# Kernel tuning notes

Measured on AMD Instinct MI355X. Metric: run time of the kernel, lower is better.

Reference implementation:

```python
import jax, jax.numpy as jnp
import numpy as np

B, D_IN, U, E = 8192, 1024, 1024, 16

def setup_inputs() -> dict:
    key = jax.random.key(0)
    k1, k2, k3, k4 = jax.random.split(key, 4)
    inputs = jax.random.normal(k1, (B, D_IN), dtype=jnp.float32)
    # type_prob: probability over entity types per example, [B, E, 1]
    tp = jax.random.uniform(k2, (B, E, 1), dtype=jnp.float32)
    type_prob = tp / jnp.sum(tp, axis=1, keepdims=True)
    # Stacked per-entity Dense params: W [E, D_IN, U], b [E, U]
    scale = 1.0 / np.sqrt(D_IN)
    W = jax.random.normal(k3, (E, D_IN, U), dtype=jnp.float32) * scale
    b = jax.random.normal(k4, (E, U), dtype=jnp.float32) * 0.01
    return {"inputs": inputs, "type_prob": type_prob, "W": W, "b": b}

def reference(inputs, type_prob, W, b):
    # Per-entity Dense, batched as one einsum: [B, E, U]
    logits = jnp.einsum('bd,edu->beu', inputs, W) + b
    probs = jax.nn.softmax(logits, axis=-1)  # softmax over wp_units, per entity
    # transpose to [B, U, E], matmul with type_prob [B, E, 1], reduce_sum last axis
    # == weighted combine over entities: [B, U]
    result = jnp.einsum('beu,be->bu', probs, type_prob[..., 0])
    return result
```

## Files before the change

kernel.cpp:

```cpp
#include <hip/hip_runtime.h>
#include <hip/hip_bf16.h>
#include <hip/hip_fp16.h>
#include <stdint.h>

typedef _Float16 f16;
typedef _Float16 f16x4 __attribute__((ext_vector_type(4)));
typedef _Float16 f16x8 __attribute__((ext_vector_type(8)));
typedef float f32x4 __attribute__((ext_vector_type(4)));

#define NB 8192
#define ND 1024
#define NU 1024
#define NE 16

__global__ __launch_bounds__(256) void k_prep(const float* __restrict__ W,
                                              f16* __restrict__ WT,
                                              const float* __restrict__ X,
                                              f16* __restrict__ Xh) {
  const int bid = blockIdx.x;
  const int t = threadIdx.x;
  if (bid < 4096) {
    __shared__ f16 tile[64][68];
    const int u0 = (bid & 15) * 64;
    const int d0 = ((bid >> 4) & 15) * 64;
    const int e = bid >> 8;
    const int r = t >> 4;
    const int c = (t & 15) << 2;
    const float* src = W + (size_t)e * ND * NU;
    f16* dst = WT + (size_t)e * NU * ND;
#pragma unroll
    for (int i = 0; i < 4; ++i) {
      const int rr = r + i * 16;
      const float4 v = *(const float4*)(src + (size_t)(d0 + rr) * NU + (u0 + c));
      tile[rr][c + 0] = (f16)v.x;
      tile[rr][c + 1] = (f16)v.y;
      tile[rr][c + 2] = (f16)v.z;
      tile[rr][c + 3] = (f16)v.w;
    }
    __syncthreads();
#pragma unroll
    for (int i = 0; i < 4; ++i) {
      const int rr = r + i * 16;
      f16x4 h;
      h[0] = tile[c + 0][rr];
      h[1] = tile[c + 1][rr];
      h[2] = tile[c + 2][rr];
      h[3] = tile[c + 3][rr];
      *(f16x4*)(dst + (size_t)(u0 + rr) * ND + (d0 + c)) = h;
    }
  } else {
    const size_t i = ((size_t)(bid - 4096) * 256 + t) * 8;
    const float4 v0 = *(const float4*)(X + i);
    const float4 v1 = *(const float4*)(X + i + 4);
    f16x8 h;
    h[0] = (f16)v0.x; h[1] = (f16)v0.y; h[2] = (f16)v0.z; h[3] = (f16)v0.w;
    h[4] = (f16)v1.x; h[5] = (f16)v1.y; h[6] = (f16)v1.z; h[7] = (f16)v1.w;
    *(f16x8*)(Xh + i) = h;
  }
}


typedef __attribute__((address_space(3))) void lds_void_t;
typedef __attribute__((address_space(1))) const void gbl_void_t;

__device__ __forceinline__ void gload16(const void* g, void* l) {
  __builtin_amdgcn_global_load_lds((gbl_void_t*)g, (lds_void_t*)l, 16, 0, 0);
}

#define WAIT_VM8() do { asm volatile("s_waitcnt vmcnt(8)" ::: "memory"); \
                        __builtin_amdgcn_sched_barrier(0); } while (0)
#define WAIT_LGKM0() do { asm volatile("s_waitcnt lgkmcnt(0)" ::: "memory"); \
                          __builtin_amdgcn_sched_barrier(0); } while (0)
#define BARR() do { asm volatile("" ::: "memory"); __builtin_amdgcn_s_barrier(); \
                    asm volatile("" ::: "memory"); } while (0)

#define STAGEA(srcp, h, kl, buf)                                                \
  {                                                                             \
    _Pragma("unroll") for (int i_ = 0; i_ < 2; ++i_) {                          \
      const unsigned s_ = i_ * 512 + t;                                         \
      const unsigned row_ = (h) * 128 + (s_ >> 3);                              \
      const unsigned sch_ = (s_ & 7) ^ (row_ & 7);                              \
      const unsigned lb_ = (unsigned)(buf) * 32768 + (h) * 16384 +              \
                           (i_ * 512 + (t & ~63u)) * 16;                        \
      gload16((srcp) + (size_t)row_ * 2048 + (size_t)(kl) * 128 + sch_ * 16,    \
              smem + lb_);                                                      \
    }                                                                           \
  }

#define LDA(mb0, buf)                                                           \
  _Pragma("unroll") for (int j_ = 0; j_ < 4; ++j_)                              \
    _Pragma("unroll") for (int ks_ = 0; ks_ < 2; ++ks_)                         \
      a[j_][ks_] = *(const f16x8*)(smem + (unsigned)(buf) * 32768 +             \
                     (wr * 128 + ((mb0) + j_) * 16 + ln) * 128 +                \
                     (((unsigned)(ks_ * 4 + g)) ^ (ln & 7u)) * 16);

#define BLOAD2(n0, kl)                                                          \
  _Pragma("unroll") for (int n_ = (n0); n_ < (n0) + 2; ++n_)                    \
    _Pragma("unroll") for (int ks_ = 0; ks_ < 2; ++ks_)                         \
      b[n_][ks_] = *(const f16x8*)(Bg + (size_t)(wc * 64 + n_ * 16 + ln) * 2048 \
                     + (size_t)(kl) * 128 + (unsigned)(ks_ * 4 + g) * 16);

#define QUAD(mb0, n0)                                                           \
  _Pragma("unroll") for (int j_ = 0; j_ < 4; ++j_)                              \
    _Pragma("unroll") for (int n_ = 0; n_ < 2; ++n_)                            \
      _Pragma("unroll") for (int ks_ = 0; ks_ < 2; ++ks_)                       \
        acc[(mb0) + j_][(n0) + n_] = __builtin_amdgcn_mfma_f32_16x16x32_f16(    \
            a[j_][ks_], b[(n0) + n_][ks_], acc[(mb0) + j_][(n0) + n_], 0, 0, 0);

__global__ __launch_bounds__(512, 2) void k_gemm_exp(const f16* __restrict__ Xc,
                                                     const f16* __restrict__ WT,
                                                     const float* __restrict__ BIAS,
                                                     f16* __restrict__ P,
                                                     float* __restrict__ S4,
                                                     int TPB, int CR) {
  __shared__ alignas(16) unsigned char smem[65536 + 4096];
  float* red = (float*)(smem + 65536);

  const int t = threadIdx.x;
  const int w = t >> 6;
  const int l = t & 63;
  const int g = l >> 4;
  const int ln = l & 15;
  const int wr = w >> 2;
  const int wc = w & 3;

  const int bid = blockIdx.x;
  const int xcd = bid & 7;
  const int i = bid >> 3;
  const int ntl = i >> 2;
  const int q = i & 3;
  const int nt = xcd * 8 + ntl;
  const int mt0 = q * TPB;

  const char* Xc0 = (const char*)Xc;
  const char* Bg = (const char*)WT + (size_t)nt * 256 * 2048;

  f32x4 acc[8][4];
#pragma unroll
  for (int mb = 0; mb < 8; ++mb)
#pragma unroll
    for (int nb = 0; nb < 4; ++nb) acc[mb][nb] = (f32x4){0.f, 0.f, 0.f, 0.f};

  f16x8 a[4][2], b[4][2];

  float bv[4];
  const float* bp = BIAS + ((size_t)(nt >> 2) << 10) + (nt & 3) * 256 + wc * 64 + ln;
#pragma unroll
  for (int nb = 0; nb < 4; ++nb) bv[nb] = bp[nb * 16];

  const int TOT = TPB * 16;

  {
    const char* Ag0 = Xc0 + (size_t)mt0 * 256 * 2048;
    STAGEA(Ag0, 0, 0, 0);
    STAGEA(Ag0, 1, 0, 0);
    __builtin_amdgcn_sched_barrier(0);
    BLOAD2(0, 0);
    BLOAD2(2, 0);
    WAIT_VM8();
    BARR();
  }

#pragma unroll 1
  for (int kt = 0; kt < TOT; ++kt) {
    const int cur = kt & 1, nxt = cur ^ 1;
    const int ti = kt >> 4;
    const bool lastk = (kt == TOT - 1);
    const int kt1 = lastk ? kt : kt + 1;
    const int t1 = kt1 >> 4, kl1 = kt1 & 15;
    const char* Ag1 = Xc0 + (size_t)(mt0 + t1) * 256 * 2048;

    LDA(0, cur);
    if (!lastk) {
      STAGEA(Ag1, 0, kl1, nxt);
      STAGEA(Ag1, 1, kl1, nxt);
    }
    __builtin_amdgcn_sched_barrier(0);
    __builtin_amdgcn_s_setprio(1);
    QUAD(0, 0);
    QUAD(0, 2);
    __builtin_amdgcn_s_setprio(0);
    LDA(4, cur);
    __builtin_amdgcn_s_setprio(1);
    QUAD(4, 0);
    __builtin_amdgcn_s_setprio(0);
    if (!lastk) BLOAD2(0, kl1);
    __builtin_amdgcn_s_setprio(1);
    QUAD(4, 2);
    __builtin_amdgcn_s_setprio(0);
    if (!lastk) {
      BLOAD2(2, kl1);
      WAIT_VM8();
    }
    BARR();

    if ((kt & 15) == 15) {
      const int mt = mt0 + ti;
      f16* Prow =
          P + (size_t)(mt * 256 + wr * 128) * 16384 + (size_t)nt * 256 + wc * 64 + ln;
#pragma unroll
      for (int mb = 0; mb < 8; ++mb) {
        float rs[4] = {0.f, 0.f, 0.f, 0.f};
#pragma unroll
        for (int nb = 0; nb < 4; ++nb) {
#pragma unroll
          for (int r = 0; r < 4; ++r) {
            const float p = __expf(acc[mb][nb][r] + bv[nb]);
            rs[r] += p;
            Prow[(size_t)(mb * 16 + g * 4 + r) * 16384 + nb * 16] = (f16)p;
            acc[mb][nb][r] = 0.f;
          }
        }
#pragma unroll
        for (int r = 0; r < 4; ++r) {
          float v = rs[r];
          v += __shfl_xor(v, 1);
          v += __shfl_xor(v, 2);
          v += __shfl_xor(v, 4);
          v += __shfl_xor(v, 8);
          if (ln == 0) red[(wr * 128 + mb * 16 + g * 4 + r) * 4 + wc] = v;
        }
      }
      WAIT_LGKM0();
      BARR();
      if (t < 256) {
        const float s =
            (red[t * 4 + 0] + red[t * 4 + 1]) + (red[t * 4 + 2] + red[t * 4 + 3]);
        S4[(size_t)nt * CR + mt * 256 + t] = s;
      }
      BARR();
    }
  }
}

__global__ __launch_bounds__(512) void k_combine(const f16* __restrict__ P,
                                                 const float* __restrict__ TP,
                                                 const float* __restrict__ S4,
                                                 float* __restrict__ OUT,
                                                 int RB, int CR) {
  __shared__ float c_s[4][16];
  const int t = threadIdx.x;
  const int blk = blockIdx.x;
  if (t < 64) {
    const int rr = t >> 4, e = t & 15;
    const int bl = blk * 4 + rr;
    float S = 0.f;
#pragma unroll
    for (int q = 0; q < 4; ++q) S += S4[(size_t)(e * 4 + q) * CR + bl];
    c_s[rr][e] = TP[(size_t)(RB + bl) * NE + e] / S;
  }
  __syncthreads();
  const int rl = t >> 7;
  const int bl = blk * 4 + rl;
  const int u0 = (t & 127) * 8;
  float acm[8] = {0.f, 0.f, 0.f, 0.f, 0.f, 0.f, 0.f, 0.f};
  const f16* Pb = P + (size_t)bl * 16384 + u0;
#pragma unroll
  for (int e = 0; e < NE; ++e) {
    const float c = c_s[rl][e];
    const f16x8 pv = *(const f16x8*)(Pb + e * 1024);
#pragma unroll
    for (int jj = 0; jj < 8; ++jj) acm[jj] += c * (float)pv[jj];
  }
  float* op = OUT + (size_t)(RB + bl) * NU + u0;
  *(float4*)(op) = (float4){acm[0], acm[1], acm[2], acm[3]};
  *(float4*)(op + 4) = (float4){acm[4], acm[5], acm[6], acm[7]};
}

#define BM 64
#define BUH 512
#define NRT 128
#define WT_BYTES ((size_t)NE * NU * ND * 2)
#define SUMS_FLOATS ((size_t)NE * NRT * 2 * 64)
#define FLG_INTS ((size_t)NE * NRT * 2)

#define LOADB(F, soff)                                   \
  {                                                      \
    const char* p_ = wtc + (soff) + vbase;               \
    F[0] = *(const f16x8*)(p_);                          \
    F[1] = *(const f16x8*)(p_ + 1 * 16 * ND * 2);        \
    F[2] = *(const f16x8*)(p_ + 2 * 16 * ND * 2);        \
    F[3] = *(const f16x8*)(p_ + 3 * 16 * ND * 2);        \
  }

#define MFMA_HALF(F, kbyte)                                                         \
  {                                                                                 \
    const f16x8 a0 = *(const f16x8*)(A_s + (ln + 0) * 2064 + g * 16 + (kbyte));     \
    const f16x8 a1 = *(const f16x8*)(A_s + (ln + 16) * 2064 + g * 16 + (kbyte));    \
    const f16x8 a2 = *(const f16x8*)(A_s + (ln + 32) * 2064 + g * 16 + (kbyte));    \
    const f16x8 a3 = *(const f16x8*)(A_s + (ln + 48) * 2064 + g * 16 + (kbyte));    \
    _Pragma("unroll") for (int n_ = 0; n_ < 4; ++n_) {                              \
      acc[0][n_] = __builtin_amdgcn_mfma_f32_16x16x32_f16(a0, F[n_], acc[0][n_], 0, 0, 0); \
      acc[1][n_] = __builtin_amdgcn_mfma_f32_16x16x32_f16(a1, F[n_], acc[1][n_], 0, 0, 0); \
      acc[2][n_] = __builtin_amdgcn_mfma_f32_16x16x32_f16(a2, F[n_], acc[2][n_], 0, 0, 0); \
      acc[3][n_] = __builtin_amdgcn_mfma_f32_16x16x32_f16(a3, F[n_], acc[3][n_], 0, 0, 0); \
    }                                                                               \
  }

__device__ __forceinline__ size_t wt_soff(int L) {
  L = (L > 511) ? 511 : L;
  return (size_t)(L >> 5) * ((size_t)NU * ND * 2) + (size_t)(L & 31) * 64;
}

__global__ __launch_bounds__(512, 2) void k_proj(const float* __restrict__ X,
                                                 const float* __restrict__ TP,
                                                 const f16* __restrict__ WT,
                                                 const float* __restrict__ BIAS,
                                                 float* __restrict__ OUT,
                                                 float* __restrict__ SUMS,
                                                 int* __restrict__ FLG) {
  __shared__ alignas(16) unsigned char lds[132096 + 4096 + 2048 + 256];
  unsigned char* A_s = lds;
  float* tp_s = (float*)(lds + 132096);
  float* reds = (float*)(lds + 132096 + 4096);
  float* sums_s = (float*)(lds + 132096 + 4096 + 2048);

  const int t = threadIdx.x;
  const int w = t >> 6;
  const int l = t & 63;
  const int g = l >> 4;
  const int ln = l & 15;
  const int bid = blockIdx.x;
  const int rt = bid >> 1;
  const int uh = bid & 1;
  const int b0 = rt * BM;
  const int c0 = uh * BUH;

#pragma unroll
  for (int i = 0; i < 32; ++i) {
    const int idx = (i * 512 + t) << 2;
    const int row = idx >> 10;
    const int col = idx & 1023;
    const float4 v = *(const float4*)(X + (size_t)(b0 + row) * ND + col);
    f16x4 h;
    h[0] = (f16)v.x; h[1] = (f16)v.y; h[2] = (f16)v.z; h[3] = (f16)v.w;
    *(f16x4*)(A_s + row * 2064 + (col << 1)) = h;
  }
  tp_s[t] = TP[(size_t)(b0 + (t >> 4)) * NE + (t & 15)];
  tp_s[512 + t] = TP[(size_t)(b0 + 32 + (t >> 4)) * NE + (t & 15)];
  __syncthreads();

  f32x4 out_acc[4][4];
#pragma unroll
  for (int m = 0; m < 4; ++m)
#pragma unroll
    for (int n = 0; n < 4; ++n) out_acc[m][n] = (f32x4){0.f, 0.f, 0.f, 0.f};

  const char* wtc = (const char*)WT;
  const unsigned vbase = ((unsigned)(c0 + w * 64 + ln) * ND + g * 8) * 2;

  f16x8 F0[4], F1[4], F2[4], F3[4];
  LOADB(F0, wt_soff(0));
  LOADB(F1, wt_soff(1));
  LOADB(F2, wt_soff(2));

  for (int e = 0; e < NE; ++e) {
    f32x4 acc[4][4];
#pragma unroll
    for (int m = 0; m < 4; ++m)
#pragma unroll
      for (int n = 0; n < 4; ++n) acc[m][n] = (f32x4){0.f, 0.f, 0.f, 0.f};

    const int Le = e * 32;
#pragma unroll 1
    for (int gi = 0; gi < 7; ++gi) {
      const int L = Le + gi * 4;
      const int kb = gi * 4 * 64;
      LOADB(F3, wt_soff(L + 3));
      MFMA_HALF(F0, kb + 0);
      LOADB(F0, wt_soff(L + 4));
      MFMA_HALF(F1, kb + 64);
      LOADB(F1, wt_soff(L + 5));
      MFMA_HALF(F2, kb + 128);
      LOADB(F2, wt_soff(L + 6));
      MFMA_HALF(F3, kb + 192);
    }
    LOADB(F3, wt_soff(Le + 31));
    MFMA_HALF(F0, 28 * 64);
    LOADB(F0, wt_soff(Le + 32));
    MFMA_HALF(F1, 29 * 64);
    LOADB(F1, wt_soff(Le + 33));
    MFMA_HALF(F2, 30 * 64);
    LOADB(F2, wt_soff(Le + 34));
    MFMA_HALF(F3, 31 * 64);

    const float* bp = BIAS + (size_t)e * NU + c0 + w * 64 + ln;
    float bv[4];
#pragma unroll
    for (int n = 0; n < 4; ++n) bv[n] = bp[n * 16];

    float rs[4][4];
#pragma unroll
    for (int m = 0; m < 4; ++m)
#pragma unroll
      for (int r = 0; r < 4; ++r) rs[m][r] = 0.f;
#pragma unroll
    for (int m = 0; m < 4; ++m)
#pragma unroll
      for (int n = 0; n < 4; ++n)
#pragma unroll
        for (int r = 0; r < 4; ++r) {
          const float p = __expf(acc[m][n][r] + bv[n]);
          acc[m][n][r] = p;
          rs[m][r] += p;
        }
#pragma unroll
    for (int m = 0; m < 4; ++m)
#pragma unroll
      for (int r = 0; r < 4; ++r) {
        float v = rs[m][r];
        v += __shfl_xor(v, 1, 64);
        v += __shfl_xor(v, 2, 64);
        v += __shfl_xor(v, 4, 64);
        v += __shfl_xor(v, 8, 64);
        rs[m][r] = v;
      }
    if (ln == 0) {
#pragma unroll
      for (int m = 0; m < 4; ++m)
#pragma unroll
        for (int r = 0; r < 4; ++r) reds[(m * 16 + g * 4 + r) * 8 + w] = rs[m][r];
    }
    __syncthreads();

    const int pairbase = (e * NRT + rt) * 2;
    float myS = 0.f;
    if (t < 64) {
      const float* rp = reds + t * 8;
      myS = ((rp[0] + rp[1]) + (rp[2] + rp[3])) + ((rp[4] + rp[5]) + (rp[6] + rp[7]));
      __hip_atomic_store(&SUMS[(size_t)(pairbase + uh) * 64 + t], myS,
                         __ATOMIC_RELAXED, __HIP_MEMORY_SCOPE_AGENT);
    }
    __syncthreads();
    if (t == 0) {
      __threadfence();
      __hip_atomic_store(&FLG[pairbase + uh], 1, __ATOMIC_RELEASE, __HIP_MEMORY_SCOPE_AGENT);
      int spin = 0;
      while (__hip_atomic_load(&FLG[pairbase + (uh ^ 1)], __ATOMIC_ACQUIRE,
                               __HIP_MEMORY_SCOPE_AGENT) == 0 &&
             spin < 400000) {
        __builtin_amdgcn_s_sleep(2);
        ++spin;
      }
    }
    __syncthreads();
    if (t < 64) {
      const float ps = __hip_atomic_load(&SUMS[(size_t)(pairbase + (uh ^ 1)) * 64 + t],
                                         __ATOMIC_RELAXED, __HIP_MEMORY_SCOPE_AGENT);
      sums_s[t] = myS + ps;
    }
    __syncthreads();

#pragma unroll
    for (int m = 0; m < 4; ++m)
#pragma unroll
      for (int r = 0; r < 4; ++r) {
        const int row = m * 16 + g * 4 + r;
        const float scale = tp_s[row * 16 + e] * __builtin_amdgcn_rcpf(sums_s[row]);
#pragma unroll
        for (int n = 0; n < 4; ++n) out_acc[m][n][r] += scale * acc[m][n][r];
      }
  }

#pragma unroll
  for (int m = 0; m < 4; ++m)
#pragma unroll
    for (int r = 0; r < 4; ++r) {
      float* op = OUT + (size_t)(b0 + m * 16 + g * 4 + r) * NU + c0 + w * 64 + ln;
#pragma unroll
      for (int n = 0; n < 4; ++n) op[n * 16] = out_acc[m][n][r];
    }
}

extern "C" void kernel_launch(void* const* d_in, const int* in_sizes, int n_in,
                              void* d_out, int out_size, void* d_ws, size_t ws_size,
                              hipStream_t stream) {
  const float* X = (const float*)d_in[0];
  const float* TP = (const float*)d_in[1];
  const float* W = (const float*)d_in[2];
  const float* BIAS = (const float*)d_in[3];
  float* OUT = (float*)d_out;

  const size_t XH_BYTES = (size_t)NB * ND * 2;
  const size_t FIXED = WT_BYTES + XH_BYTES;

  int CR = 0;
  for (int cr = NB; cr >= 1024; cr >>= 1) {
    const size_t need = FIXED + (size_t)cr * 16384 * 2 + (size_t)cr * 64 * 4;
    if (ws_size >= need) { CR = cr; break; }
  }

  if (CR > 0) {
    f16* WT = (f16*)d_ws;
    f16* Xh = (f16*)((char*)d_ws + WT_BYTES);
    float* S4 = (float*)((char*)d_ws + FIXED);
    f16* P = (f16*)((char*)d_ws + FIXED + (size_t)CR * 64 * 4);

    k_prep<<<dim3(8192), dim3(256), 0, stream>>>(W, WT, X, Xh);

    const int MT = CR / 256;
    const int TPB = MT / 4;
    const int nch = NB / CR;
    for (int ch = 0; ch < nch; ++ch) {
      const int RB = ch * CR;
      k_gemm_exp<<<dim3(256), dim3(512), 0, stream>>>(
          (const f16*)((const char*)Xh + (size_t)RB * ND * 2), WT, BIAS, P, S4, TPB, CR);
      k_combine<<<dim3(CR / 4), dim3(512), 0, stream>>>(P, TP, S4, OUT, RB, CR);
    }
  } else {
    f16* WT = (f16*)d_ws;
    float* SUMS = (float*)((char*)d_ws + WT_BYTES);
    int* FLG = (int*)((char*)d_ws + WT_BYTES + SUMS_FLOATS * 4);

    hipMemsetAsync(FLG, 0, FLG_INTS * sizeof(int), stream);
    k_prep<<<dim3(4096), dim3(256), 0, stream>>>(W, WT, X, nullptr);
    k_proj<<<dim3(256), dim3(512), 0, stream>>>(X, TP, WT, BIAS, OUT, SUMS, FLG);
  }
}
```

Baseline: 461.8 us.

## Stage B tiles through LDS with deeper ping-pong pipeline and interleaved barriers

B (weight) tiles are now staged into LDS with direct global-to-LDS loads instead of being read straight from global memory into registers. The LDS buffer doubles to 128KB and the main loop is unrolled by two with ping-pong buffers. Loads are prefetched two k-steps ahead and split into chunks interleaved between MFMA quads, separated by barriers. This aims to hide global latency and get coalesced B reads, but it adds many barriers per step and enough LDS use to limit occupancy.

```diff
diff --git a/kernel.cpp b/kernel.cpp
--- a/kernel.cpp
+++ b/kernel.cpp
@@ -67,38 +67,31 @@
   __builtin_amdgcn_global_load_lds((gbl_void_t*)g, (lds_void_t*)l, 16, 0, 0);
 }
 
-#define WAIT_VM8() do { asm volatile("s_waitcnt vmcnt(8)" ::: "memory"); \
+#define WAIT_VM6() do { asm volatile("s_waitcnt vmcnt(6)" ::: "memory"); \
+                        __builtin_amdgcn_sched_barrier(0); } while (0)
+#define WAIT_VM0() do { asm volatile("s_waitcnt vmcnt(0)" ::: "memory"); \
                         __builtin_amdgcn_sched_barrier(0); } while (0)
 #define WAIT_LGKM0() do { asm volatile("s_waitcnt lgkmcnt(0)" ::: "memory"); \
                           __builtin_amdgcn_sched_barrier(0); } while (0)
 #define BARR() do { asm volatile("" ::: "memory"); __builtin_amdgcn_s_barrier(); \
                     asm volatile("" ::: "memory"); } while (0)
 
-#define STAGEA(srcp, h, kl, buf)                                                \
-  {                                                                             \
-    _Pragma("unroll") for (int i_ = 0; i_ < 2; ++i_) {                          \
-      const unsigned s_ = i_ * 512 + t;                                         \
-      const unsigned row_ = (h) * 128 + (s_ >> 3);                              \
-      const unsigned sch_ = (s_ & 7) ^ (row_ & 7);                              \
-      const unsigned lb_ = (unsigned)(buf) * 32768 + (h) * 16384 +              \
-                           (i_ * 512 + (t & ~63u)) * 16;                        \
-      gload16((srcp) + (size_t)row_ * 2048 + (size_t)(kl) * 128 + sch_ * 16,    \
-              smem + lb_);                                                      \
-    }                                                                           \
-  }
-
-#define LDA(mb0, buf)                                                           \
-  _Pragma("unroll") for (int j_ = 0; j_ < 4; ++j_)                              \
-    _Pragma("unroll") for (int ks_ = 0; ks_ < 2; ++ks_)                         \
-      a[j_][ks_] = *(const f16x8*)(smem + (unsigned)(buf) * 32768 +             \
-                     (wr * 128 + ((mb0) + j_) * 16 + ln) * 128 +                \
-                     (((unsigned)(ks_ * 4 + g)) ^ (ln & 7u)) * 16);
-
-#define BLOAD2(n0, kl)                                                          \
-  _Pragma("unroll") for (int n_ = (n0); n_ < (n0) + 2; ++n_)                    \
-    _Pragma("unroll") for (int ks_ = 0; ks_ < 2; ++ks_)                         \
-      b[n_][ks_] = *(const f16x8*)(Bg + (size_t)(wc * 64 + n_ * 16 + ln) * 2048 \
-                     + (size_t)(kl) * 128 + (unsigned)(ks_ * 4 + g) * 16);
+#define STG(srcp, op, h, kb, BUF)                                               \
+  { _Pragma("unroll") for (int i_ = 0; i_ < 2; ++i_)                            \
+      gload16((srcp) + (h) * 262144 + (size_t)(kb) + sOff[i_],                  \
+              smem + ((BUF) * 65536 + (op) * 32768 + (h) * 16384) + dOff[i_]); }
+
+#define LDA2(mb0, CB)                                                           \
+  _Pragma("unroll") for (int j_ = 0; j_ < 4; ++j_) {                            \
+    a[j_][0] = *(const f16x8*)(smem + A0b[CB] + ((mb0) + j_) * 2048);           \
+    a[j_][1] = *(const f16x8*)(smem + A1b[CB] + ((mb0) + j_) * 2048);           \
+  }
+
+#define LDB2(CB)                                                                \
+  _Pragma("unroll") for (int n_ = 0; n_ < 4; ++n_) {                            \
+    b[n_][0] = *(const f16x8*)(smem + B0b[CB] + n_ * 2048);                     \
+    b[n_][1] = *(const f16x8*)(smem + B1b[CB] + n_ * 2048);                     \
+  }
 
 #define QUAD(mb0, n0)                                                           \
   _Pragma("unroll") for (int j_ = 0; j_ < 4; ++j_)                              \
@@ -107,14 +100,49 @@
         acc[(mb0) + j_][(n0) + n_] = __builtin_amdgcn_mfma_f32_16x16x32_f16(    \
             a[j_][ks_], b[(n0) + n_][ks_], acc[(mb0) + j_][(n0) + n_], 0, 0, 0);
 
+#define KBODY(ktv, CB)                                                          \
+  {                                                                             \
+    const int kt_ = (ktv);                                                      \
+    const bool lastT_ = ((kt_ >> 4) == TPB - 1);                                \
+    const bool lastk_ = (kt_ == TOT - 1);                                       \
+    const bool sk14_ = lastT_ && ((kt_ & 15) >= 14);                            \
+    const int kt1_ = lastk_ ? kt_ : kt_ + 1;                                    \
+    const char* Ag1_ = Xc0 + (size_t)(mt0 + (kt1_ >> 4)) * 524288;              \
+    const int kb1_ = (kt1_ & 15) * 128;                                         \
+    const int kt2_ = (kt_ + 2 < TOT) ? kt_ + 2 : kt_;                           \
+    const char* Ag2_ = Xc0 + (size_t)(mt0 + (kt2_ >> 4)) * 524288;              \
+    const int kb2_ = (kt2_ & 15) * 128;                                         \
+    if (lastk_) { WAIT_VM0(); BARR(); }                                         \
+    LDA2(0, CB);                                                                \
+    LDB2(CB);                                                                   \
+    if (!lastk_) STG(Ag1_, 0, 1, kb1_, (CB) ^ 1);                               \
+    BARR();                                                                     \
+    __builtin_amdgcn_s_setprio(1); QUAD(0, 0); __builtin_amdgcn_s_setprio(0);   \
+    BARR();                                                                     \
+    if (!sk14_) STG(Bg, 1, 0, kb2_, CB);                                        \
+    BARR();                                                                     \
+    __builtin_amdgcn_s_setprio(1); QUAD(0, 2); __builtin_amdgcn_s_setprio(0);   \
+    BARR();                                                                     \
+    LDA2(4, CB);                                                                \
+    if (!sk14_) STG(Bg, 1, 1, kb2_, CB);                                        \
+    BARR();                                                                     \
+    __builtin_amdgcn_s_setprio(1); QUAD(4, 2); __builtin_amdgcn_s_setprio(0);   \
+    BARR();                                                                     \
+    if (!sk14_) STG(Ag2_, 0, 0, kb2_, CB);                                      \
+    BARR();                                                                     \
+    __builtin_amdgcn_s_setprio(1); QUAD(4, 0); __builtin_amdgcn_s_setprio(0);   \
+    if (!lastk_) WAIT_VM6();                                                    \
+    BARR();                                                                     \
+  }
+
 __global__ __launch_bounds__(512, 2) void k_gemm_exp(const f16* __restrict__ Xc,
                                                      const f16* __restrict__ WT,
                                                      const float* __restrict__ BIAS,
                                                      f16* __restrict__ P,
                                                      float* __restrict__ S4,
                                                      int TPB, int CR) {
-  __shared__ alignas(16) unsigned char smem[65536 + 4096];
-  float* red = (float*)(smem + 65536);
+  __shared__ alignas(16) unsigned char smem[131072 + 4096];
+  float* red = (float*)(smem + 131072);
 
   const int t = threadIdx.x;
   const int w = t >> 6;
@@ -133,7 +161,25 @@
   const int mt0 = q * TPB;
 
   const char* Xc0 = (const char*)Xc;
-  const char* Bg = (const char*)WT + (size_t)nt * 256 * 2048;
+  const char* Bg = (const char*)WT + (size_t)nt * 524288;
+
+  const unsigned aRow = (unsigned)(wr * 128 + ln) * 128;
+  const unsigned bRow = 32768u + (unsigned)(wc >> 1) * 16384 +
+                        (unsigned)((wc & 1) * 64 + ln) * 128;
+  const unsigned x0 = (unsigned)(g ^ (ln & 7)) * 16;
+  const unsigned x1 = (unsigned)((4 + g) ^ (ln & 7)) * 16;
+  const unsigned A0b[2] = {aRow + x0, aRow + x0 + 65536u};
+  const unsigned A1b[2] = {aRow + x1, aRow + x1 + 65536u};
+  const unsigned B0b[2] = {bRow + x0, bRow + x0 + 65536u};
+  const unsigned B1b[2] = {bRow + x1, bRow + x1 + 65536u};
+
+  unsigned sOff[2], dOff[2];
+#pragma unroll
+  for (int i_ = 0; i_ < 2; ++i_) {
+    const unsigned s_ = i_ * 512 + t;
+    sOff[i_] = (s_ >> 3) * 2048 + (((s_ & 7) ^ ((s_ >> 3) & 7)) * 16);
+    dOff[i_] = (i_ * 512 + (t & ~63u)) * 16;
+  }
 
   f32x4 acc[8][4];
 #pragma unroll
@@ -151,51 +197,25 @@
   const int TOT = TPB * 16;
 
   {
-    const char* Ag0 = Xc0 + (size_t)mt0 * 256 * 2048;
-    STAGEA(Ag0, 0, 0, 0);
-    STAGEA(Ag0, 1, 0, 0);
-    __builtin_amdgcn_sched_barrier(0);
-    BLOAD2(0, 0);
-    BLOAD2(2, 0);
-    WAIT_VM8();
+    const char* Ag0 = Xc0 + (size_t)mt0 * 524288;
+    STG(Ag0, 0, 0, 0, 0);
+    STG(Ag0, 0, 1, 0, 0);
+    STG(Bg, 1, 0, 0, 0);
+    STG(Bg, 1, 1, 0, 0);
+    STG(Bg, 1, 0, 128, 1);
+    STG(Bg, 1, 1, 128, 1);
+    STG(Ag0, 0, 0, 128, 1);
+    WAIT_VM6();
     BARR();
   }
 
 #pragma unroll 1
-  for (int kt = 0; kt < TOT; ++kt) {
-    const int cur = kt & 1, nxt = cur ^ 1;
-    const int ti = kt >> 4;
-    const bool lastk = (kt == TOT - 1);
-    const int kt1 = lastk ? kt : kt + 1;
-    const int t1 = kt1 >> 4, kl1 = kt1 & 15;
-    const char* Ag1 = Xc0 + (size_t)(mt0 + t1) * 256 * 2048;
-
-    LDA(0, cur);
-    if (!lastk) {
-      STAGEA(Ag1, 0, kl1, nxt);
-      STAGEA(Ag1, 1, kl1, nxt);
-    }
-    __builtin_amdgcn_sched_barrier(0);
-    __builtin_amdgcn_s_setprio(1);
-    QUAD(0, 0);
-    QUAD(0, 2);
-    __builtin_amdgcn_s_setprio(0);
-    LDA(4, cur);
-    __builtin_amdgcn_s_setprio(1);
-    QUAD(4, 0);
-    __builtin_amdgcn_s_setprio(0);
-    if (!lastk) BLOAD2(0, kl1);
-    __builtin_amdgcn_s_setprio(1);
-    QUAD(4, 2);
-    __builtin_amdgcn_s_setprio(0);
-    if (!lastk) {
-      BLOAD2(2, kl1);
-      WAIT_VM8();
-    }
-    BARR();
-
-    if ((kt & 15) == 15) {
-      const int mt = mt0 + ti;
+  for (int kp = 0; kp < (TOT >> 1); ++kp) {
+    KBODY(kp * 2, 0);
+    KBODY(kp * 2 + 1, 1);
+
+    if (((kp * 2 + 1) & 15) == 15) {
+      const int mt = mt0 + ((kp * 2 + 1) >> 4);
       f16* Prow =
           P + (size_t)(mt * 256 + wr * 128) * 16384 + (size_t)nt * 256 + wc * 64 + ln;
 #pragma unroll
```

New measurement: 376.4 us. 1.23x faster.
